# Optimization experiments

Measured on AMD Instinct MI355X. Metric: run time of the kernel, lower is better.

Reference implementation:

```python
import jax, jax.numpy as jnp
import numpy as np

N = 100_000      # nodes
E_HALF = 1_600_000  # undirected edges (mirrored -> 3.2M directed)
D = 128          # feature dim
K = 1            # k-MIS hop parameter


def setup_inputs() -> dict:
    key = jax.random.key(0)
    k1, k2, k3, k4, k5 = jax.random.split(key, 5)
    x = jax.random.normal(k1, (N, D), dtype=jnp.float32)
    src = jax.random.randint(k2, (E_HALF,), 0, N)
    dst = jax.random.randint(k3, (E_HALF,), 0, N)
    # symmetric edge list (undirected graph), as k-MIS coverage assumes
    edge_index = jnp.stack([jnp.concatenate([src, dst]),
                            jnp.concatenate([dst, src])])
    ea = jax.random.uniform(k4, (E_HALF,), dtype=jnp.float32)
    edge_attr = jnp.concatenate([ea, ea])
    # RandomScorer: score is a uniform random vector over nodes
    score = jax.random.uniform(k5, (N,), dtype=jnp.float32)
    return {"x": x, "edge_index": edge_index, "edge_attr": edge_attr, "score": score}


def _scatter_min(values, index, n, fill):
    return jnp.full((n,), fill, dtype=values.dtype).at[index].min(values)


def maximal_k_independent_set(row, col, n, k, rank):
    # Iteratively: propagate min rank k hops; nodes equal to their own
    # (uncovered) min rank join the MIS; mark their k-hop neighborhood covered.
    mis = jnp.zeros(n, dtype=bool)
    mask = jnp.zeros(n, dtype=bool)
    min_rank = rank
    while not bool(mask.all()):
        for _ in range(k):
            mn = _scatter_min(min_rank[row], col, n, n)
            min_rank = jnp.minimum(mn, min_rank)
        mis = mis | ((rank == min_rank) & ~mask)
        mask = mask | mis
        for _ in range(k):
            nb = jnp.zeros(n, dtype=bool).at[col].max(mask[row])
            mask = mask | nb
        min_rank = jnp.where(mask, n, rank)
    return mis


def cluster_k_mis(mis, row, col, n, k, rank):
    # assign every node to the MIS node of minimum rank within k hops
    min_rank = jnp.where(mis, rank, n)
    for _ in range(k):
        mn = _scatter_min(min_rank[row], col, n, n)
        min_rank = jnp.minimum(mn, min_rank)
    _, clusters = jnp.unique(min_rank, return_inverse=True)  # sorted uniques
    perm = jnp.argsort(rank[mis])  # sorted-rank position -> index into x[mis]
    return perm[clusters.ravel()]


def reference(x, edge_index, edge_attr, score):
    n = x.shape[0]
    row, col = edge_index[0], edge_index[1]
    # Greedy ordering: rank = inverse permutation of argsort(score)
    rank = jnp.argsort(jnp.argsort(score))
    mis = maximal_k_independent_set(row, col, n, K, rank)
    cluster = cluster_k_mis(mis, row, col, n, K, rank)
    # sparse_reduce_adj: map edges into cluster space, coalesce with sum
    pairs = jnp.stack([cluster[row], cluster[col]], axis=1)  # [E,2]
    uk, inv = jnp.unique(pairs, axis=0, return_inverse=True)
    vals = jax.ops.segment_sum(edge_attr, inv.ravel(), num_segments=uk.shape[0])
    r2, c2 = uk[:, 0], uk[:, 1]
    keep = r2 != c2  # remove_self_loops
    edge_index_out = jnp.stack([r2[keep], c2[keep]])
    edge_attr_out = vals[keep]
    x_out = x[jnp.nonzero(mis)[0]]  # reduce_x=None -> select MIS node features
    return x_out, edge_index_out, edge_attr_out, cluster, mis, score
```

## Files before the change

### kernel.cpp

```cpp
#include <hip/hip_runtime.h>
#include <stdint.h>

#define RTILE 4096
#define ROUNDS 10


__global__ void k_init_counters(int* counters){
  int t = threadIdx.x;
  counters[t] = 0;
  if (t == 7) counters[7] = 1;
}
__global__ void k_init_nodes(int* mis, int N){
  int v = blockIdx.x*blockDim.x + threadIdx.x;
  if (v < N) mis[v]=0;
}
__global__ void k_zero_vals(float* vals, int E){
  int i = blockIdx.x*blockDim.x + threadIdx.x;
  if (i < E) vals[i]=0.f;
}

__global__ void k_score_key(const float* score, unsigned* keys, unsigned* pay, int N){
  int i = blockIdx.x*blockDim.x+threadIdx.x;
  if (i<N){
    unsigned b = __float_as_uint(score[i]);
    b ^= ((int)b < 0) ? 0xFFFFFFFFu : 0x80000000u;
    keys[i]=b; pay[i]=(unsigned)i;
  }
}
__global__ void k_rank_build(const unsigned* pay, int* rank, int* pm, int N){
  int p = blockIdx.x*blockDim.x+threadIdx.x;
  if (p<N){ int v = (int)pay[p]; rank[v]=p; pm[v]=p; }
}
__global__ void k_make_colrow(const int* __restrict__ row, const int* __restrict__ col,
                              unsigned* __restrict__ keys, unsigned* __restrict__ pay, int E){
  int e = blockIdx.x*blockDim.x+threadIdx.x;
  if (e<E){ keys[e]=(unsigned)col[e]; pay[e]=(unsigned)row[e]; }
}

template<typename K, int TILE>
__global__ void k_radix_hist(const K* __restrict__ keys, int n, int shift,
                             unsigned* __restrict__ ghist, int numBlocks, const int* gate){
  if (*gate==0) return;
  __shared__ unsigned h[512];
  int t=threadIdx.x, b=blockIdx.x;
  h[t]=0; h[t+256]=0; __syncthreads();
  int base = b*TILE;
  for (int j=t; j<TILE; j+=256){
    int i = base+j;
    if (i<n){
      unsigned d = (unsigned)((keys[i]>>shift)&(K)511);
      atomicAdd(&h[d],1u);
    }
  }
  __syncthreads();
  ghist[(size_t)t*numBlocks + b] = h[t];
  ghist[(size_t)(t+256)*numBlocks + b] = h[t+256];
}

template<typename K, int TILE>
__global__ void k_radix_scatter(const K* __restrict__ keysIn, const unsigned* __restrict__ payIn,
                                K* __restrict__ keysOut, unsigned* __restrict__ payOut,
                                int n, int shift, const unsigned* __restrict__ gbase,
                                int numBlocks, const int* gate){
  if (*gate==0) return;
  __shared__ unsigned lbase[512];
  __shared__ unsigned carry[512];
  __shared__ unsigned ss[256];
  __shared__ K        skey[TILE];
  __shared__ unsigned spay[TILE];
  int t=threadIdx.x, b=blockIdx.x;
  int base = b*TILE;
  int cnt = min(TILE, n-base);
  carry[t]=0; carry[t+256]=0; __syncthreads();
  for (int c=0;c<TILE/256;++c){
    int i = base+c*256+t;
    if (i<n){
      unsigned d = (unsigned)((keysIn[i]>>shift)&(K)511);
      atomicAdd(&carry[d],1u);
    }
  }
  __syncthreads();
  unsigned a0=carry[2*t], a1=carry[2*t+1];
  ss[t]=a0+a1; __syncthreads();
  for (int off=1; off<256; off<<=1){
    unsigned x = (t>=off)? ss[t-off]:0u; __syncthreads();
    ss[t]+=x; __syncthreads();
  }
  unsigned excl = t? ss[t-1]:0u;
  __syncthreads();
  lbase[2*t]=excl;      lbase[2*t+1]=excl+a0;
  carry[2*t]=excl;      carry[2*t+1]=excl+a0;
  __syncthreads();
  int lane = t&63, wave = t>>6;
  for (int c=0;c<TILE/256;++c){
    int i = base + c*256 + t;
    bool valid = i<n;
    K k = valid ? keysIn[i] : (K)0;
    unsigned pay = valid ? payIn[i] : 0u;
    unsigned d = (unsigned)((k>>shift)&(K)511);
    unsigned off=0;
    for (int w=0; w<4; ++w){
      if (wave==w){
        unsigned long long m = __ballot(valid);
        #pragma unroll
        for (int bit=0; bit<9; ++bit){
          unsigned long long bb = __ballot((d>>bit)&1u);
          m &= ((d>>bit)&1u) ? bb : ~bb;
        }
        int lr = __popcll(m & ((1ull<<lane)-1ull));
        unsigned cb = carry[d];
        off = cb + (unsigned)lr;
        if (valid && lr==0) carry[d] = cb + (unsigned)__popcll(m);
      }
      __syncthreads();
    }
    if (valid){ skey[off]=k; spay[off]=pay; }
  }
  __syncthreads();
  for (int c=0;c<TILE/256;++c){
    int j = c*256 + t;
    if (j<cnt){
      K k = skey[j];
      unsigned d = (unsigned)((k>>shift)&(K)511);
      unsigned gpos = gbase[(size_t)d*numBlocks + b] + ((unsigned)j - lbase[d]);
      keysOut[gpos]=k; payOut[gpos]=spay[j];
    }
  }
}

__global__ void k_scan_single(unsigned* data, int n, unsigned* total, const int* gate){
  if (*gate==0) return;
  __shared__ unsigned sh[1024];
  __shared__ unsigned carry;
  int t=threadIdx.x;
  if (t==0) carry=0;
  __syncthreads();
  for (int base=0; base<n; base+=4096){
    unsigned v[4]; unsigned s=0;
    int i0 = base + t*4;
    #pragma unroll
    for (int j=0;j<4;j++){ int i=i0+j; v[j] = (i<n)?data[i]:0u; s+=v[j]; }
    sh[t]=s; __syncthreads();
    for (int off=1; off<1024; off<<=1){
      unsigned x = (t>=off)? sh[t-off]:0u; __syncthreads();
      sh[t]+=x; __syncthreads();
    }
    unsigned excl = (t?sh[t-1]:0u) + carry;
    #pragma unroll
    for (int j=0;j<4;j++){ int i=i0+j; if(i<n){ unsigned o=v[j]; data[i]=excl; excl+=o; } }
    unsigned tot = sh[1023];
    __syncthreads();
    if (t==0) carry += tot;
    __syncthreads();
  }
  if (total && t==0) *total = carry;
}

__global__ void k_scan_partials(const unsigned* __restrict__ in, unsigned* __restrict__ bsums,
                                int n, const int* gate){
  if (*gate==0) return;
  __shared__ unsigned sh[256];
  int b=blockIdx.x, t=threadIdx.x;
  long base = (long)b*RTILE + (long)t*16;
  unsigned s=0;
  #pragma unroll
  for (int j=0;j<16;j++){ long i=base+j; if(i<n) s+=in[i]; }
  sh[t]=s; __syncthreads();
  for (int off=128; off>0; off>>=1){ if(t<off) sh[t]+=sh[t+off]; __syncthreads(); }
  if (t==0) bsums[b]=sh[0];
}
__global__ void k_scan_final(const unsigned* __restrict__ in, unsigned* __restrict__ out,
                             const unsigned* __restrict__ bsums, int n, const int* gate){
  if (*gate==0) return;
  __shared__ unsigned sh[256];
  int b=blockIdx.x, t=threadIdx.x;
  long base = (long)b*RTILE + (long)t*16;
  unsigned v[16]; unsigned s=0;
  #pragma unroll
  for (int j=0;j<16;j++){ long i=base+j; v[j]=(i<n)?in[i]:0u; s+=v[j]; }
  sh[t]=s; __syncthreads();
  for (int off=1; off<256; off<<=1){
    unsigned x=(t>=off)?sh[t-off]:0u; __syncthreads(); sh[t]+=x; __syncthreads();
  }
  unsigned run=(t?sh[t-1]:0u)+bsums[b];
  #pragma unroll
  for (int j=0;j<16;j++){ long i=base+j; if(i<n){ unsigned o=v[j]; out[i]=run; run+=o; } }
}

__global__ void k_build_off(const unsigned* __restrict__ scol, int* __restrict__ off, int E, int N){
  int i = blockIdx.x*blockDim.x+threadIdx.x;
  if (i>=E) return;
  int c = (int)scol[i];
  int p = (i==0) ? -1 : (int)scol[i-1];
  for (int v=p+1; v<=c; ++v) off[v]=i;
  if (i==E-1){ for (int v=c+1; v<=N; ++v) off[v]=E; }
}

__global__ void k_round1(const int* __restrict__ off, const int* __restrict__ nbr,
                         const int* __restrict__ pm, int* __restrict__ mis,
                         int* __restrict__ maskA, int N, const int* gate){
  if (*gate==0) return;
  int v = blockIdx.x*blockDim.x+threadIdx.x;
  if (v>=N) return;
  int p = pm[v];
  if (p == N){ maskA[v]=1; return; }
  int m = p;
  int s=off[v], e=off[v+1];
  for (int j=s; j<e; ++j){ int u=nbr[j]; m = min(m, pm[u]); }
  int nm = (m == p);
  if (nm) mis[v]=1;
  maskA[v] = nm;
}
__global__ void k_round2(const int* __restrict__ off, const int* __restrict__ nbr,
                         const int* __restrict__ maskA, int* __restrict__ pm,
                         int N, int* cnt, const int* gate){
  if (*gate==0) return;
  int v = blockIdx.x*blockDim.x+threadIdx.x;
  int um = 0;
  if (v<N){
    int mk = maskA[v];
    int s=off[v], e=off[v+1];
    for (int j=s; j<e && !mk; ++j) mk |= maskA[nbr[j]];
    if (mk) pm[v] = N;
    um = !mk;
  }
  unsigned long long bm = __ballot(um);
  if ((threadIdx.x&63)==0 && bm) atomicAdd(cnt, (int)__popcll(bm));
}

__global__ void k_cl_init(const int* rank, const int* mis, int* pm, int N){
  int v = blockIdx.x*blockDim.x+threadIdx.x;
  if (v<N) pm[v] = mis[v] ? rank[v] : N;
}
__global__ void k_cl_gather(const int* __restrict__ off, const int* __restrict__ nbr,
                            const int* __restrict__ pm, int* __restrict__ mn, int N){
  int v = blockIdx.x*blockDim.x+threadIdx.x;
  if (v>=N) return;
  int m = pm[v];
  int s=off[v], e=off[v+1];
  for (int j=s; j<e; ++j) m = min(m, pm[nbr[j]]);
  mn[v] = m;
}
__global__ void k_copy_u32(const int* in, unsigned* out, int N){
  int v = blockIdx.x*blockDim.x+threadIdx.x;
  if (v<N) out[v]=(unsigned)in[v];
}
__global__ void k_cl_map(const int* rank, const int* mis, const unsigned* cidx,
                         int* map, int* rmax, int N){
  int v = blockIdx.x*blockDim.x+threadIdx.x;
  if (v<N && mis[v]){ map[rank[v]] = (int)cidx[v]; atomicMax(rmax, rank[v]); }
}
__global__ void k_cl_cluster(const int* mn, const int* map, const int* rmax, int* cluster, int N){
  int v = blockIdx.x*blockDim.x+threadIdx.x;
  if (v<N){
    int mr = mn[v];
    if (mr >= N) mr = *rmax;
    cluster[v] = map[mr];
  }
}
__global__ void k_gather_x(const float4* __restrict__ x, float4* __restrict__ out,
                           const int* __restrict__ mis, const unsigned* __restrict__ cidx,
                           int N, int D4){
  int t = blockIdx.x*blockDim.x+threadIdx.x;
  int v = t / D4, q = t - v*D4;
  if (v<N && mis[v]) out[(size_t)cidx[v]*D4 + q] = x[(size_t)v*D4 + q];
}

__global__ void k_set_gates(int* counters){
  int M = counters[1];
  int sh = (M<=1) ? 1 : (32-__clz((unsigned)(M-1)));
  int kb = 2*sh;
  int npass = 1 + (9<kb) + (18<kb) + (27<kb);
  counters[36] = sh;
  counters[32] = 1;
  counters[33] = (9  < kb);
  counters[34] = (18 < kb);
  counters[35] = (27 < kb);
  counters[37] = npass & 1;
}
__global__ void k_pair_key(const int* __restrict__ row, const int* __restrict__ col,
                           const int* __restrict__ cluster, const float* __restrict__ attr,
                           unsigned long long* __restrict__ keys, unsigned* __restrict__ pay,
                           const int* __restrict__ counters, int E){
  int e = blockIdx.x*blockDim.x+threadIdx.x;
  if (e<E){
    int sh = counters[36];
    unsigned a = (unsigned)cluster[row[e]], b=(unsigned)cluster[col[e]];
    keys[e] = ((unsigned long long)a<<sh) | b;
    pay[e] = __float_as_uint(attr[e]);
  }
}
__global__ void k_flags(const unsigned long long* __restrict__ keyA,
                        const unsigned long long* __restrict__ keyB,
                        unsigned* __restrict__ fhead, unsigned* __restrict__ fkeep,
                        const int* __restrict__ counters, int E){
  const unsigned long long* keys = counters[37] ? keyB : keyA;
  int i = blockIdx.x*blockDim.x+threadIdx.x;
  if (i<E){
    int sh = counters[36];
    unsigned long long k = keys[i];
    unsigned head = (i==0) || (k != keys[i-1]);
    unsigned a=(unsigned)(k>>sh), b=(unsigned)(k & ((1ull<<sh)-1ull));
    fhead[i]=head;
    fkeep[i]=(head && a!=b) ? 1u : 0u;
  }
}
__global__ void k_acc_seg(const unsigned long long* __restrict__ keyA,
                          const unsigned long long* __restrict__ keyB,
                          const unsigned* __restrict__ payA, const unsigned* __restrict__ payB,
                          const unsigned* __restrict__ excl1,
                          float* __restrict__ vals, const int* __restrict__ counters, int E){
  const unsigned long long* keys = counters[37] ? keyB : keyA;
  const unsigned* pay = counters[37] ? payB : payA;
  int i = blockIdx.x*blockDim.x+threadIdx.x;
  int lane = threadIdx.x & 63;
  bool valid = i < E;
  unsigned long long k = valid ? keys[i] : ~0ull;
  float v = valid ? __uint_as_float(pay[i]) : 0.f;
  #pragma unroll
  for (int off=1; off<64; off<<=1){
    float o = __shfl_up(v, off);
    unsigned long long ko = __shfl_up(k, off);
    if (lane >= off && ko == k) v += o;
  }
  if (valid){
    unsigned long long knext = (i+1<E) ? keys[i+1] : ~0ull;
    if (lane==63 || k != knext){
      unsigned head = (i==0) || (keys[i-1] != k);
      atomicAdd(&vals[excl1[i] + head - 1u], v);
    }
  }
}
__global__ void k_write_edges(const unsigned long long* __restrict__ keyA,
                              const unsigned long long* __restrict__ keyB,
                              const unsigned* __restrict__ excl1, const unsigned* __restrict__ excl2,
                              const float* __restrict__ vals, float* __restrict__ out,
                              const int* __restrict__ counters, int E, int D){
  const unsigned long long* keys = counters[37] ? keyB : keyA;
  int i = blockIdx.x*blockDim.x+threadIdx.x;
  if (i<E){
    int sh = counters[36];
    int head=(i==0)||(keys[i]!=keys[i-1]);
    unsigned a=(unsigned)(keys[i]>>sh), b=(unsigned)(keys[i] & ((1ull<<sh)-1ull));
    if (head && a!=b){
      unsigned opos = excl2[i];
      int M = counters[1], Ep = counters[3];
      size_t off = (size_t)M*D;
      out[off + opos] = (float)a;
      out[off + (size_t)Ep + opos] = (float)b;
      out[off + 2*(size_t)Ep + opos] = vals[excl1[i]];
    }
  }
}
__global__ void k_write_nodes(const int* __restrict__ cluster, const int* __restrict__ mis,
                              const float* __restrict__ score, float* __restrict__ out,
                              const int* __restrict__ counters, int N, int D){
  int v = blockIdx.x*blockDim.x+threadIdx.x;
  if (v<N){
    int M=counters[1], Ep=counters[3];
    size_t off = (size_t)M*D + 3*(size_t)Ep;
    out[off + v] = (float)cluster[v];
    out[off + (size_t)N + v] = mis[v] ? 1.f : 0.f;
    out[off + 2*(size_t)N + v] = score[v];
  }
}

extern "C" void kernel_launch(void* const* d_in, const int* in_sizes, int n_in,
                              void* d_out, int out_size, void* d_ws, size_t ws_size,
                              hipStream_t stream){
  const float* x     = (const float*)d_in[0];
  const int*   ei    = (const int*)d_in[1];
  const float* attr  = (const float*)d_in[2];
  const float* score = (const float*)d_in[3];
  int N = in_sizes[3];
  int E = in_sizes[2];
  int D = in_sizes[0]/N;
  const int* row = ei;
  const int* col = ei + E;
  float* out = (float*)d_out;

  char* p = (char*)d_ws;
  auto alloc = [&](size_t bytes)->char*{ char* r=p; p += ((bytes+255)/256)*256; return r; };
  unsigned long long* keyA = (unsigned long long*)alloc((size_t)E*8);
  unsigned long long* keyB = (unsigned long long*)alloc((size_t)E*8);
  unsigned* payA  = (unsigned*)alloc((size_t)E*4);
  unsigned* payB  = (unsigned*)alloc((size_t)E*4);
  unsigned* scanA = (unsigned*)alloc((size_t)E*4);
  unsigned* scanB = (unsigned*)alloc((size_t)E*4);
  float*    vals  = (float*)alloc((size_t)E*4);
  int* csr_row = (int*)alloc((size_t)E*4);
  unsigned* off= (unsigned*)alloc((size_t)(N+1)*4);
  int* rank   = (int*)alloc((size_t)N*4);
  int* pm     = (int*)alloc((size_t)N*4);
  int* mis    = (int*)alloc((size_t)N*4);
  int* maskA  = (int*)alloc((size_t)N*4);
  int* mnArr  = (int*)alloc((size_t)N*4);
  int* map    = (int*)alloc((size_t)N*4);
  unsigned* cidx = (unsigned*)alloc((size_t)N*4);
  int* cluster= (int*)alloc((size_t)N*4);
  int* counters=(int*)alloc(256*4);
  int Be = (E + RTILE-1)/RTILE;
  int Bn1k = (N + 1023)/1024;
  unsigned* ghist = (unsigned*)alloc((size_t)512*Be*4);
  unsigned* bsums = (unsigned*)alloc(4096*4);

  int nbN = (N+255)/256, nbE = (E+255)/256;
  const int* ON = counters+7;

  auto big_scan = [&](unsigned* data, int n, unsigned* total, const int* gate){
    int B = (n + RTILE-1)/RTILE;
    k_scan_partials<<<B,256,0,stream>>>(data,bsums,n,gate);
    k_scan_single<<<1,1024,0,stream>>>(bsums,B,total,gate);
    k_scan_final<<<B,256,0,stream>>>(data,data,bsums,n,gate);
  };

  k_init_counters<<<1,256,0,stream>>>(counters);
  k_init_nodes<<<nbN,256,0,stream>>>(mis,N);
  k_zero_vals<<<nbE,256,0,stream>>>(vals,E);

  k_make_colrow<<<nbE,256,0,stream>>>(row,col,(unsigned*)keyA,payA,E);
  k_radix_hist<unsigned,RTILE><<<Be,256,0,stream>>>((unsigned*)keyA,E,0,ghist,Be,ON);
  big_scan(ghist,512*Be,nullptr,ON);
  k_radix_scatter<unsigned,RTILE><<<Be,256,0,stream>>>((unsigned*)keyA,payA,(unsigned*)keyB,payB,E,0,ghist,Be,ON);
  k_radix_hist<unsigned,RTILE><<<Be,256,0,stream>>>((unsigned*)keyB,E,9,ghist,Be,ON);
  big_scan(ghist,512*Be,nullptr,ON);
  k_radix_scatter<unsigned,RTILE><<<Be,256,0,stream>>>((unsigned*)keyB,payB,scanA,(unsigned*)csr_row,E,9,ghist,Be,ON);
  k_build_off<<<nbE,256,0,stream>>>(scanA,(int*)off,E,N);

  k_score_key<<<nbN,256,0,stream>>>(score,(unsigned*)keyA,payA,N);
  {
    unsigned *ki=(unsigned*)keyA,*ko=(unsigned*)keyB,*pi=payA,*po=payB;
    for (int pass=0; pass<4; ++pass){
      int shift = pass*9;
      k_radix_hist<unsigned,1024><<<Bn1k,256,0,stream>>>(ki,N,shift,ghist,Bn1k,ON);
      big_scan(ghist,512*Bn1k,nullptr,ON);
      k_radix_scatter<unsigned,1024><<<Bn1k,256,0,stream>>>(ki,pi,ko,po,N,shift,ghist,Bn1k,ON);
      unsigned* tk=ki; ki=ko; ko=tk; unsigned* tp=pi; pi=po; po=tp;
    }
    k_rank_build<<<nbN,256,0,stream>>>(pi, rank, pm, N);
  }

  for (int r=0; r<ROUNDS; ++r){
    const int* gate = (r==0) ? ON : (counters + 8 + r - 1);
    int* cnt = counters + 8 + r;
    k_round1<<<nbN,256,0,stream>>>((const int*)off,csr_row,pm,mis,maskA,N,gate);
    k_round2<<<nbN,256,0,stream>>>((const int*)off,csr_row,maskA,pm,N,cnt,gate);
  }

  k_cl_init<<<nbN,256,0,stream>>>(rank,mis,pm,N);
  k_cl_gather<<<nbN,256,0,stream>>>((const int*)off,csr_row,pm,mnArr,N);
  k_copy_u32<<<nbN,256,0,stream>>>(mis,cidx,N);
  big_scan(cidx,N,(unsigned*)(counters+1),ON);
  k_cl_map<<<nbN,256,0,stream>>>(rank,mis,cidx,map,counters+4,N);
  k_cl_cluster<<<nbN,256,0,stream>>>(mnArr,map,counters+4,cluster,N);
  k_gather_x<<<(N*(D/4)+255)/256,256,0,stream>>>((const float4*)x,(float4*)out,mis,cidx,N,D/4);

  k_set_gates<<<1,1,0,stream>>>(counters);
  k_pair_key<<<nbE,256,0,stream>>>(row,col,cluster,attr,keyA,payA,counters,E);
  {
    unsigned long long *ki=keyA,*ko=keyB; unsigned *pi=payA,*po=payB;
    for (int pass=0; pass<4; ++pass){
      int shift = pass*9;
      const int* g = counters + 32 + pass;
      k_radix_hist<unsigned long long,RTILE><<<Be,256,0,stream>>>(ki,E,shift,ghist,Be,g);
      big_scan(ghist,512*Be,nullptr,g);
      k_radix_scatter<unsigned long long,RTILE><<<Be,256,0,stream>>>(ki,pi,ko,po,E,shift,ghist,Be,g);
      unsigned long long* tk=ki; ki=ko; ko=tk; unsigned* tp=pi; pi=po; po=tp;
    }
    k_flags<<<nbE,256,0,stream>>>(keyA,keyB,scanA,scanB,counters,E);
    big_scan(scanA,E,(unsigned*)(counters+2),ON);
    big_scan(scanB,E,(unsigned*)(counters+3),ON);
    k_acc_seg<<<nbE,256,0,stream>>>(keyA,keyB,payA,payB,scanA,vals,counters,E);
    k_write_edges<<<nbE,256,0,stream>>>(keyA,keyB,scanA,scanB,vals,out,counters,E,D);
  }
  k_write_nodes<<<nbN,256,0,stream>>>(cluster,mis,score,out,counters,N,D);
}
```

Measured before the change: 1.024 ms.

## Rework radix scatter with per-wave histograms and fuse dual flag scans into one 64-bit scan

The radix scatter kernel now keeps keys and payloads in registers, builds per-wave histograms, and replaces the serialized four-wave ballot loop with wave-local atomic offset reservation. It also reuses one shared-memory buffer for keys and then payloads, which cuts LDS use. Separately, the head and keep flags are packed into one 64-bit word so a single scan replaces two 32-bit scans. This trades wider 64-bit scan traffic for fewer launches and passes. The 64-bit total written at counters+2 also overlaps counters+3, relying on the packed high half landing there.

```diff
diff --git a/kernel.cpp b/kernel.cpp
--- a/kernel.cpp
+++ b/kernel.cpp
@@ -58,133 +58,161 @@
 }
 
 template<typename K, int TILE>
-__global__ void k_radix_scatter(const K* __restrict__ keysIn, const unsigned* __restrict__ payIn,
-                                K* __restrict__ keysOut, unsigned* __restrict__ payOut,
-                                int n, int shift, const unsigned* __restrict__ gbase,
-                                int numBlocks, const int* gate){
-  if (*gate==0) return;
+__global__ __launch_bounds__(256)
+void k_radix_scatter(const K* __restrict__ keysIn, const unsigned* __restrict__ payIn,
+                     K* __restrict__ keysOut, unsigned* __restrict__ payOut,
+                     int n, int shift, const unsigned* __restrict__ gbase,
+                     int numBlocks, const int* gate){
+  if (*gate==0) return;
+  constexpr int G = TILE/256;
+  constexpr int SEG = TILE/4;
+  __shared__ __align__(16) char smem[(size_t)TILE*sizeof(K)];
+  K* skey = (K*)smem;
+  unsigned* spay = (unsigned*)smem;
+  __shared__ unsigned whist[4][512];
   __shared__ unsigned lbase[512];
-  __shared__ unsigned carry[512];
   __shared__ unsigned ss[256];
-  __shared__ K        skey[TILE];
-  __shared__ unsigned spay[TILE];
   int t=threadIdx.x, b=blockIdx.x;
+  int lane = t&63, wave = t>>6;
   int base = b*TILE;
-  int cnt = min(TILE, n-base);
-  carry[t]=0; carry[t+256]=0; __syncthreads();
-  for (int c=0;c<TILE/256;++c){
-    int i = base+c*256+t;
-    if (i<n){
-      unsigned d = (unsigned)((keysIn[i]>>shift)&(K)511);
-      atomicAdd(&carry[d],1u);
-    }
-  }
-  __syncthreads();
-  unsigned a0=carry[2*t], a1=carry[2*t+1];
-  ss[t]=a0+a1; __syncthreads();
+  int tilecnt = min(TILE, n-base);
+  int segBase = base + wave*SEG;
+
+  for (int j=lane; j<512; j+=64) whist[wave][j]=0;
+  K keys[G]; unsigned pays[G];
+  for (int g=0; g<G; ++g){
+    int i = segBase + g*64 + lane;
+    bool valid = i<n;
+    keys[g] = valid ? keysIn[i] : (K)0;
+    pays[g] = valid ? payIn[i] : 0u;
+    if (valid){
+      unsigned d = (unsigned)((keys[g]>>shift)&(K)511);
+      atomicAdd(&whist[wave][d],1u);
+    }
+  }
+  __syncthreads();
+
+  unsigned h0[4], h1[4], u0=0, u1=0;
+  #pragma unroll
+  for (int w=0;w<4;++w){ h0[w]=whist[w][2*t];   u0+=h0[w];
+                         h1[w]=whist[w][2*t+1]; u1+=h1[w]; }
+  ss[t]=u0+u1; __syncthreads();
   for (int off=1; off<256; off<<=1){
-    unsigned x = (t>=off)? ss[t-off]:0u; __syncthreads();
+    unsigned x=(t>=off)?ss[t-off]:0u; __syncthreads();
     ss[t]+=x; __syncthreads();
   }
   unsigned excl = t? ss[t-1]:0u;
-  __syncthreads();
-  lbase[2*t]=excl;      lbase[2*t+1]=excl+a0;
-  carry[2*t]=excl;      carry[2*t+1]=excl+a0;
-  __syncthreads();
-  int lane = t&63, wave = t>>6;
-  for (int c=0;c<TILE/256;++c){
-    int i = base + c*256 + t;
+  lbase[2*t]=excl; lbase[2*t+1]=excl+u0;
+  unsigned c0=excl, c1=excl+u0;
+  #pragma unroll
+  for (int w=0;w<4;++w){ whist[w][2*t]=c0;   c0+=h0[w];
+                         whist[w][2*t+1]=c1; c1+=h1[w]; }
+  __syncthreads();
+
+  unsigned offs[G];
+  for (int g=0; g<G; ++g){
+    int i = segBase + g*64 + lane;
     bool valid = i<n;
-    K k = valid ? keysIn[i] : (K)0;
-    unsigned pay = valid ? payIn[i] : 0u;
-    unsigned d = (unsigned)((k>>shift)&(K)511);
-    unsigned off=0;
-    for (int w=0; w<4; ++w){
-      if (wave==w){
-        unsigned long long m = __ballot(valid);
-        #pragma unroll
-        for (int bit=0; bit<9; ++bit){
-          unsigned long long bb = __ballot((d>>bit)&1u);
-          m &= ((d>>bit)&1u) ? bb : ~bb;
-        }
-        int lr = __popcll(m & ((1ull<<lane)-1ull));
-        unsigned cb = carry[d];
-        off = cb + (unsigned)lr;
-        if (valid && lr==0) carry[d] = cb + (unsigned)__popcll(m);
-      }
-      __syncthreads();
-    }
-    if (valid){ skey[off]=k; spay[off]=pay; }
-  }
-  __syncthreads();
-  for (int c=0;c<TILE/256;++c){
-    int j = c*256 + t;
-    if (j<cnt){
-      K k = skey[j];
-      unsigned d = (unsigned)((k>>shift)&(K)511);
-      unsigned gpos = gbase[(size_t)d*numBlocks + b] + ((unsigned)j - lbase[d]);
-      keysOut[gpos]=k; payOut[gpos]=spay[j];
-    }
-  }
-}
-
-__global__ void k_scan_single(unsigned* data, int n, unsigned* total, const int* gate){
-  if (*gate==0) return;
-  __shared__ unsigned sh[1024];
-  __shared__ unsigned carry;
+    unsigned d = (unsigned)((keys[g]>>shift)&(K)511);
+    unsigned long long m = __ballot(valid);
+    #pragma unroll
+    for (int bit=0; bit<9; ++bit){
+      unsigned long long bb = __ballot((d>>bit)&1u);
+      m &= ((d>>bit)&1u) ? bb : ~bb;
+    }
+    if (valid){
+      int lr = __popcll(m & ((1ull<<lane)-1ull));
+      int leader = __ffsll((unsigned long long)m)-1;
+      unsigned old=0;
+      if (lr==0) old = atomicAdd(&whist[wave][d], (unsigned)__popcll(m));
+      old = __shfl(old, leader);
+      unsigned o = old + (unsigned)lr;
+      skey[o]=keys[g]; offs[g]=o;
+    }
+  }
+  __syncthreads();
+
+  unsigned gpos_[G];
+  for (int c=0;c<G;++c){
+    int j=c*256+t;
+    if (j<tilecnt){
+      K k=skey[j];
+      unsigned d=(unsigned)((k>>shift)&(K)511);
+      unsigned gp = gbase[(size_t)d*numBlocks + b] + ((unsigned)j - lbase[d]);
+      keysOut[gp]=k; gpos_[c]=gp;
+    }
+  }
+  __syncthreads();
+  for (int g=0; g<G; ++g){
+    int i = segBase + g*64 + lane;
+    if (i<n) spay[offs[g]]=pays[g];
+  }
+  __syncthreads();
+  for (int c=0;c<G;++c){
+    int j=c*256+t;
+    if (j<tilecnt) payOut[gpos_[c]] = spay[j];
+  }
+}
+
+template<typename T>
+__global__ void k_scan_single(T* data, int n, T* total, const int* gate){
+  if (*gate==0) return;
+  __shared__ T sh[1024];
+  __shared__ T carry;
   int t=threadIdx.x;
-  if (t==0) carry=0;
+  if (t==0) carry=(T)0;
   __syncthreads();
   for (int base=0; base<n; base+=4096){
-    unsigned v[4]; unsigned s=0;
+    T v[4]; T s=(T)0;
     int i0 = base + t*4;
     #pragma unroll
-    for (int j=0;j<4;j++){ int i=i0+j; v[j] = (i<n)?data[i]:0u; s+=v[j]; }
+    for (int j=0;j<4;j++){ int i=i0+j; v[j] = (i<n)?data[i]:(T)0; s+=v[j]; }
     sh[t]=s; __syncthreads();
     for (int off=1; off<1024; off<<=1){
-      unsigned x = (t>=off)? sh[t-off]:0u; __syncthreads();
+      T x = (t>=off)? sh[t-off]:(T)0; __syncthreads();
       sh[t]+=x; __syncthreads();
     }
-    unsigned excl = (t?sh[t-1]:0u) + carry;
+    T excl = (t?sh[t-1]:(T)0) + carry;
     #pragma unroll
-    for (int j=0;j<4;j++){ int i=i0+j; if(i<n){ unsigned o=v[j]; data[i]=excl; excl+=o; } }
-    unsigned tot = sh[1023];
+    for (int j=0;j<4;j++){ int i=i0+j; if(i<n){ T o=v[j]; data[i]=excl; excl+=o; } }
+    T tot = sh[1023];
     __syncthreads();
     if (t==0) carry += tot;
     __syncthreads();
   }
   if (total && t==0) *total = carry;
 }
-
-__global__ void k_scan_partials(const unsigned* __restrict__ in, unsigned* __restrict__ bsums,
+template<typename T>
+__global__ void k_scan_partials(const T* __restrict__ in, T* __restrict__ bsums,
                                 int n, const int* gate){
   if (*gate==0) return;
-  __shared__ unsigned sh[256];
+  __shared__ T sh[256];
   int b=blockIdx.x, t=threadIdx.x;
   long base = (long)b*RTILE + (long)t*16;
-  unsigned s=0;
+  T s=(T)0;
   #pragma unroll
   for (int j=0;j<16;j++){ long i=base+j; if(i<n) s+=in[i]; }
   sh[t]=s; __syncthreads();
   for (int off=128; off>0; off>>=1){ if(t<off) sh[t]+=sh[t+off]; __syncthreads(); }
   if (t==0) bsums[b]=sh[0];
 }
-__global__ void k_scan_final(const unsigned* __restrict__ in, unsigned* __restrict__ out,
-                             const unsigned* __restrict__ bsums, int n, const int* gate){
-  if (*gate==0) return;
-  __shared__ unsigned sh[256];
+template<typename T>
+__global__ void k_scan_final(const T* __restrict__ in, T* __restrict__ out,
+                             const T* __restrict__ bsums, int n, const int* gate){
+  if (*gate==0) return;
+  __shared__ T sh[256];
   int b=blockIdx.x, t=threadIdx.x;
   long base = (long)b*RTILE + (long)t*16;
-  unsigned v[16]; unsigned s=0;
+  T v[16]; T s=(T)0;
   #pragma unroll
-  for (int j=0;j<16;j++){ long i=base+j; v[j]=(i<n)?in[i]:0u; s+=v[j]; }
+  for (int j=0;j<16;j++){ long i=base+j; v[j]=(i<n)?in[i]:(T)0; s+=v[j]; }
   sh[t]=s; __syncthreads();
   for (int off=1; off<256; off<<=1){
-    unsigned x=(t>=off)?sh[t-off]:0u; __syncthreads(); sh[t]+=x; __syncthreads();
-  }
-  unsigned run=(t?sh[t-1]:0u)+bsums[b];
+    T x=(t>=off)?sh[t-off]:(T)0; __syncthreads(); sh[t]+=x; __syncthreads();
+  }
+  T run=(t?sh[t-1]:(T)0)+bsums[b];
   #pragma unroll
-  for (int j=0;j<16;j++){ long i=base+j; if(i<n){ unsigned o=v[j]; out[i]=run; run+=o; } }
+  for (int j=0;j<16;j++){ long i=base+j; if(i<n){ T o=v[j]; out[i]=run; run+=o; } }
 }
 
 __global__ void k_build_off(const unsigned* __restrict__ scol, int* __restrict__ off, int E, int N){
@@ -292,7 +320,7 @@
 }
 __global__ void k_flags(const unsigned long long* __restrict__ keyA,
                         const unsigned long long* __restrict__ keyB,
-                        unsigned* __restrict__ fhead, unsigned* __restrict__ fkeep,
+                        unsigned long long* __restrict__ fcomb,
                         const int* __restrict__ counters, int E){
   const unsigned long long* keys = counters[37] ? keyB : keyA;
   int i = blockIdx.x*blockDim.x+threadIdx.x;
@@ -301,14 +329,14 @@
     unsigned long long k = keys[i];
     unsigned head = (i==0) || (k != keys[i-1]);
     unsigned a=(unsigned)(k>>sh), b=(unsigned)(k & ((1ull<<sh)-1ull));
-    fhead[i]=head;
-    fkeep[i]=(head && a!=b) ? 1u : 0u;
+    unsigned keep = (head && a!=b) ? 1u : 0u;
+    fcomb[i] = ((unsigned long long)keep<<32) | head;
   }
 }
 __global__ void k_acc_seg(const unsigned long long* __restrict__ keyA,
                           const unsigned long long* __restrict__ keyB,
                           const unsigned* __restrict__ payA, const unsigned* __restrict__ payB,
-                          const unsigned* __restrict__ excl1,
+                          const unsigned long long* __restrict__ fcomb,
                           float* __restrict__ vals, const int* __restrict__ counters, int E){
   const unsigned long long* keys = counters[37] ? keyB : keyA;
   const unsigned* pay = counters[37] ? payB : payA;
@@ -327,13 +355,14 @@
     unsigned long long knext = (i+1<E) ? keys[i+1] : ~0ull;
     if (lane==63 || k != knext){
       unsigned head = (i==0) || (keys[i-1] != k);
-      atomicAdd(&vals[excl1[i] + head - 1u], v);
+      unsigned e1 = (unsigned)fcomb[i];
+      atomicAdd(&vals[e1 + head - 1u], v);
     }
   }
 }
 __global__ void k_write_edges(const unsigned long long* __restrict__ keyA,
                               const unsigned long long* __restrict__ keyB,
-                              const unsigned* __restrict__ excl1, const unsigned* __restrict__ excl2,
+                              const unsigned long long* __restrict__ fcomb,
                               const float* __restrict__ vals, float* __restrict__ out,
                               const int* __restrict__ counters, int E, int D){
   const unsigned long long* keys = counters[37] ? keyB : keyA;
@@ -343,12 +372,13 @@
     int head=(i==0)||(keys[i]!=keys[i-1]);
     unsigned a=(unsigned)(keys[i]>>sh), b=(unsigned)(keys[i] & ((1ull<<sh)-1ull));
     if (head && a!=b){
-      unsigned opos = excl2[i];
+      unsigned long long sc = fcomb[i];
+      unsigned opos = (unsigned)(sc>>32);
       int M = counters[1], Ep = counters[3];
       size_t off = (size_t)M*D;
       out[off + opos] = (float)a;
       out[off + (size_t)Ep + opos] = (float)b;
-      out[off + 2*(size_t)Ep + opos] = vals[excl1[i]];
+      out[off + 2*(size_t)Ep + opos] = vals[(unsigned)sc];
     }
   }
 }
@@ -363,6 +393,15 @@
     out[off + (size_t)N + v] = mis[v] ? 1.f : 0.f;
     out[off + 2*(size_t)N + v] = score[v];
   }
+}
+
+template<typename T>
+static void big_scan_t(T* data, int n, T* total, const int* gate, void* bsums_raw, hipStream_t stream){
+  int B = (n + RTILE-1)/RTILE;
+  T* bsums = (T*)bsums_raw;
+  k_scan_partials<T><<<B,256,0,stream>>>(data,bsums,n,gate);
+  k_scan_single<T><<<1,1024,0,stream>>>(bsums,B,total,gate);
+  k_scan_final<T><<<B,256,0,stream>>>(data,data,bsums,n,gate);
 }
 
 extern "C" void kernel_launch(void* const* d_in, const int* in_sizes, int n_in,
@@ -386,7 +425,7 @@
   unsigned* payA  = (unsigned*)alloc((size_t)E*4);
   unsigned* payB  = (unsigned*)alloc((size_t)E*4);
   unsigned* scanA = (unsigned*)alloc((size_t)E*4);
-  unsigned* scanB = (unsigned*)alloc((size_t)E*4);
+  unsigned long long* fcomb = (unsigned long long*)alloc((size_t)E*8);
   float*    vals  = (float*)alloc((size_t)E*4);
   int* csr_row = (int*)alloc((size_t)E*4);
   unsigned* off= (unsigned*)alloc((size_t)(N+1)*4);
@@ -402,17 +441,10 @@
   int Be = (E + RTILE-1)/RTILE;
   int Bn1k = (N + 1023)/1024;
   unsigned* ghist = (unsigned*)alloc((size_t)512*Be*4);
-  unsigned* bsums = (unsigned*)alloc(4096*4);
+  void* bsums = (void*)alloc(4096*8);
 
   int nbN = (N+255)/256, nbE = (E+255)/256;
   const int* ON = counters+7;
-
-  auto big_scan = [&](unsigned* data, int n, unsigned* total, const int* gate){
-    int B = (n + RTILE-1)/RTILE;
-    k_scan_partials<<<B,256,0,stream>>>(data,bsums,n,gate);
-    k_scan_single<<<1,1024,0,stream>>>(bsums,B,total,gate);
-    k_scan_final<<<B,256,0,stream>>>(data,data,bsums,n,gate);
-  };
 
   k_init_counters<<<1,256,0,stream>>>(counters);
   k_init_nodes<<<nbN,256,0,stream>>>(mis,N);
@@ -420,10 +452,10 @@
 
   k_make_colrow<<<nbE,256,0,stream>>>(row,col,(unsigned*)keyA,payA,E);
   k_radix_hist<unsigned,RTILE><<<Be,256,0,stream>>>((unsigned*)keyA,E,0,ghist,Be,ON);
-  big_scan(ghist,512*Be,nullptr,ON);
+  big_scan_t<unsigned>(ghist,512*Be,nullptr,ON,bsums,stream);
   k_radix_scatter<unsigned,RTILE><<<Be,256,0,stream>>>((unsigned*)keyA,payA,(unsigned*)keyB,payB,E,0,ghist,Be,ON);
   k_radix_hist<unsigned,RTILE><<<Be,256,0,stream>>>((unsigned*)keyB,E,9,ghist,Be,ON);
-  big_scan(ghist,512*Be,nullptr,ON);
+  big_scan_t<unsigned>(ghist,512*Be,nullptr,ON,bsums,stream);
   k_radix_scatter<unsigned,RTILE><<<Be,256,0,stream>>>((unsigned*)keyB,payB,scanA,(unsigned*)csr_row,E,9,ghist,Be,ON);
   k_build_off<<<nbE,256,0,stream>>>(scanA,(int*)off,E,N);
 
@@ -433,7 +465,7 @@
     for (int pass=0; pass<4; ++pass){
       int shift = pass*9;
       k_radix_hist<unsigned,1024><<<Bn1k,256,0,stream>>>(ki,N,shift,ghist,Bn1k,ON);
-      big_scan(ghist,512*Bn1k,nullptr,ON);
+      big_scan_t<unsigned>(ghist,512*Bn1k,nullptr,ON,bsums,stream);
       k_radix_scatter<unsigned,1024><<<Bn1k,256,0,stream>>>(ki,pi,ko,po,N,shift,ghist,Bn1k,ON);
       unsigned* tk=ki; ki=ko; ko=tk; unsigned* tp=pi; pi=po; po=tp;
     }
@@ -450,7 +482,7 @@
   k_cl_init<<<nbN,256,0,stream>>>(rank,mis,pm,N);
   k_cl_gather<<<nbN,256,0,stream>>>((const int*)off,csr_row,pm,mnArr,N);
   k_copy_u32<<<nbN,256,0,stream>>>(mis,cidx,N);
-  big_scan(cidx,N,(unsigned*)(counters+1),ON);
+  big_scan_t<unsigned>(cidx,N,(unsigned*)(counters+1),ON,bsums,stream);
   k_cl_map<<<nbN,256,0,stream>>>(rank,mis,cidx,map,counters+4,N);
   k_cl_cluster<<<nbN,256,0,stream>>>(mnArr,map,counters+4,cluster,N);
   k_gather_x<<<(N*(D/4)+255)/256,256,0,stream>>>((const float4*)x,(float4*)out,mis,cidx,N,D/4);
@@ -463,15 +495,14 @@
       int shift = pass*9;
       const int* g = counters + 32 + pass;
       k_radix_hist<unsigned long long,RTILE><<<Be,256,0,stream>>>(ki,E,shift,ghist,Be,g);
-      big_scan(ghist,512*Be,nullptr,g);
+      big_scan_t<unsigned>(ghist,512*Be,nullptr,g,bsums,stream);
       k_radix_scatter<unsigned long long,RTILE><<<Be,256,0,stream>>>(ki,pi,ko,po,E,shift,ghist,Be,g);
       unsigned long long* tk=ki; ki=ko; ko=tk; unsigned* tp=pi; pi=po; po=tp;
     }
-    k_flags<<<nbE,256,0,stream>>>(keyA,keyB,scanA,scanB,counters,E);
-    big_scan(scanA,E,(unsigned*)(counters+2),ON);
-    big_scan(scanB,E,(unsigned*)(counters+3),ON);
-    k_acc_seg<<<nbE,256,0,stream>>>(keyA,keyB,payA,payB,scanA,vals,counters,E);
-    k_write_edges<<<nbE,256,0,stream>>>(keyA,keyB,scanA,scanB,vals,out,counters,E,D);
+    k_flags<<<nbE,256,0,stream>>>(keyA,keyB,fcomb,counters,E);
+    big_scan_t<unsigned long long>(fcomb,E,(unsigned long long*)(counters+2),ON,bsums,stream);
+    k_acc_seg<<<nbE,256,0,stream>>>(keyA,keyB,payA,payB,fcomb,vals,counters,E);
+    k_write_edges<<<nbE,256,0,stream>>>(keyA,keyB,fcomb,vals,out,counters,E,D);
   }
   k_write_nodes<<<nbN,256,0,stream>>>(cluster,mis,score,out,counters,N,D);
 }
```

After: 878.2 us. -14.2%, faster.
